# Kernel tuning notes

Hardware: AMD Instinct MI355X
Metric: run time of the kernel (lower is better)

## Reference

```python
import jax, jax.numpy as jnp
import numpy as np

DIM = 6
HID = 8
N_UT = DIM * (DIM - 1) // 2  # 15


def setup_inputs() -> dict:
    key = jax.random.key(0)
    ks = jax.random.split(key, 13)
    B, T = 256, 4096
    x = jax.random.normal(ks[0], (B, T, DIM), dtype=jnp.float32)

    def kaiming(k, fan_out, fan_in):
        std = np.sqrt(2.0 / fan_in)
        return jax.random.normal(k, (fan_out, fan_in), dtype=jnp.float32) * std

    inp = {
        "x": x,
        "W_in": kaiming(ks[1], HID, DIM),
        "b_in": jnp.zeros((HID,), jnp.float32),
        "W1": kaiming(ks[2], HID, HID), "b1": jnp.zeros((HID,), jnp.float32),
        "W2": kaiming(ks[3], HID, HID), "b2": jnp.zeros((HID,), jnp.float32),
        "W3": kaiming(ks[4], HID, HID), "b3": jnp.zeros((HID,), jnp.float32),
        "W4": kaiming(ks[5], HID, HID), "b4": jnp.zeros((HID,), jnp.float32),
        "W_out": kaiming(ks[6], N_UT, HID),
        "b_out": jnp.zeros((N_UT,), jnp.float32),
    }
    return inp


def reference(x, W_in, b_in, W1, b1, W2, b2, W3, b3, W4, b4, W_out, b_out):
    B, T, dim = x.shape
    xf = x.reshape(B * T, dim)
    sp = jax.nn.softplus
    y = sp(xf @ W_in.T + b_in)
    y = sp(y @ W1.T + b1)
    y = sp(y @ W2.T + b2)
    y = sp(y @ W3.T + b3)
    y = sp(y @ W4.T + b4)
    ut = y @ W_out.T + b_out  # [N, dim*(dim-1)/2]
    iu, ju = jnp.triu_indices(dim, k=1)  # row-major order matches torch loop
    L = jnp.zeros((B * T, dim, dim), dtype=x.dtype)
    L = L.at[:, iu, ju].set(ut)
    L = L.at[:, ju, iu].set(-ut)
    return L.reshape(B, T, dim, dim)
```

## Files before the change

### kernel.cpp

```cpp
#include <hip/hip_runtime.h>

#define DEV_INLINE __device__ __forceinline__

DEV_INLINE float softplus_f(float v) {
    return fmaxf(v, 0.0f) + __logf(1.0f + __expf(-fabsf(v)));
}

__global__ __launch_bounds__(256) void pb_kernel(
    const float* __restrict__ x,
    const float* __restrict__ W_in, const float* __restrict__ b_in,
    const float* __restrict__ W1,   const float* __restrict__ b1,
    const float* __restrict__ W2,   const float* __restrict__ b2,
    const float* __restrict__ W3,   const float* __restrict__ b3,
    const float* __restrict__ W4,   const float* __restrict__ b4,
    const float* __restrict__ W_out,const float* __restrict__ b_out,
    float* __restrict__ out, int n_rows)
{
    __shared__ float4 sbuf[256 * 9];

    const int tid = threadIdx.x;
    const int row_raw = blockIdx.x * 256 + tid;
    const int row = row_raw < n_rows ? row_raw : n_rows - 1;

    const float2* xv = (const float2*)(x + (size_t)row * 6);
    float2 p0 = xv[0], p1 = xv[1], p2 = xv[2];
    const float xin[6] = { p0.x, p0.y, p1.x, p1.y, p2.x, p2.y };

    float y[8];
    #pragma unroll
    for (int o = 0; o < 8; ++o) {
        float acc = b_in[o];
        #pragma unroll
        for (int i = 0; i < 6; ++i)
            acc = fmaf(W_in[o * 6 + i], xin[i], acc);
        y[o] = softplus_f(acc);
    }

    const float* Ws[4] = { W1, W2, W3, W4 };
    const float* bs[4] = { b1, b2, b3, b4 };
    #pragma unroll
    for (int l = 0; l < 4; ++l) {
        const float* __restrict__ W = Ws[l];
        const float* __restrict__ b = bs[l];
        float t[8];
        #pragma unroll
        for (int o = 0; o < 8; ++o) {
            float acc = b[o];
            #pragma unroll
            for (int i = 0; i < 8; ++i)
                acc = fmaf(W[o * 8 + i], y[i], acc);
            t[o] = softplus_f(acc);
        }
        #pragma unroll
        for (int o = 0; o < 8; ++o) y[o] = t[o];
    }

    float u[15];
    #pragma unroll
    for (int o = 0; o < 15; ++o) {
        float acc = b_out[o];
        #pragma unroll
        for (int i = 0; i < 8; ++i)
            acc = fmaf(W_out[o * 8 + i], y[i], acc);
        u[o] = acc;
    }

    float L[36];
    #pragma unroll
    for (int i = 0; i < 36; ++i) L[i] = 0.0f;
    {
        int k = 0;
        #pragma unroll
        for (int i = 0; i < 6; ++i) {
            #pragma unroll
            for (int j = i + 1; j < 6; ++j) {
                L[i * 6 + j] = u[k];
                L[j * 6 + i] = -u[k];
                ++k;
            }
        }
    }

    #pragma unroll
    for (int m = 0; m < 9; ++m)
        sbuf[tid * 9 + m] = make_float4(L[4 * m + 0], L[4 * m + 1],
                                        L[4 * m + 2], L[4 * m + 3]);

    __syncthreads();

    float4* dst = (float4*)out + (size_t)blockIdx.x * (256 * 9);
    const long long total_f4 = (long long)n_rows * 9;
    #pragma unroll
    for (int q = 0; q < 9; ++q) {
        const int idx = q * 256 + tid;
        const long long gidx = (long long)blockIdx.x * (256 * 9) + idx;
        if (gidx < total_f4)
            dst[idx] = sbuf[idx];
    }
}

extern "C" void kernel_launch(void* const* d_in, const int* in_sizes, int n_in,
                              void* d_out, int out_size, void* d_ws, size_t ws_size,
                              hipStream_t stream) {
    const float* x     = (const float*)d_in[0];
    const float* W_in  = (const float*)d_in[1];
    const float* b_in  = (const float*)d_in[2];
    const float* W1    = (const float*)d_in[3];
    const float* b1    = (const float*)d_in[4];
    const float* W2    = (const float*)d_in[5];
    const float* b2    = (const float*)d_in[6];
    const float* W3    = (const float*)d_in[7];
    const float* b3    = (const float*)d_in[8];
    const float* W4    = (const float*)d_in[9];
    const float* b4    = (const float*)d_in[10];
    const float* W_out = (const float*)d_in[11];
    const float* b_out = (const float*)d_in[12];
    float* out = (float*)d_out;

    const int n_rows = in_sizes[0] / 6;
    const int block = 256;
    const int grid = (n_rows + block - 1) / block;

    hipLaunchKernelGGL(pb_kernel, dim3(grid), dim3(block), 0, stream,
                       x, W_in, b_in, W1, b1, W2, b2, W3, b3, W4, b4,
                       W_out, b_out, out, n_rows);
}
```

Baseline: 197.2 us.

## Use per-wave LDS staging, nontemporal stores, and native exp2/log softplus

Splits the shared staging buffer into one slice per wavefront, so each wave transposes its own 64 rows and only waits on its own LDS writes instead of a block-wide barrier. The output is written with nontemporal stores so the large write stream does not pollute the cache. Softplus now calls the hardware exp2/log builtins with base conversion to avoid the extra work in __expf/__logf. The bounds check on the output is removed, which assumes the row count is a multiple of 256. Relying on an s_waitcnt with no barrier assumes intra-wave lockstep, which is fragile.

```diff
diff --git a/kernel.cpp b/kernel.cpp
--- a/kernel.cpp
+++ b/kernel.cpp
@@ -2,8 +2,16 @@
 
 #define DEV_INLINE __device__ __forceinline__
 
+typedef float vfloat4 __attribute__((ext_vector_type(4)));
+
 DEV_INLINE float softplus_f(float v) {
+#if __has_builtin(__builtin_amdgcn_logf) && __has_builtin(__builtin_amdgcn_exp2f)
+    float e = __builtin_amdgcn_exp2f(fabsf(v) * -1.44269504f);
+    float l = __builtin_amdgcn_logf(1.0f + e);
+    return fmaf(0.69314718f, l, fmaxf(v, 0.0f));
+#else
     return fmaxf(v, 0.0f) + __logf(1.0f + __expf(-fabsf(v)));
+#endif
 }
 
 __global__ __launch_bounds__(256) void pb_kernel(
@@ -16,9 +24,11 @@
     const float* __restrict__ W_out,const float* __restrict__ b_out,
     float* __restrict__ out, int n_rows)
 {
-    __shared__ float4 sbuf[256 * 9];
+    __shared__ vfloat4 sbuf[4][64 * 9];
 
-    const int tid = threadIdx.x;
+    const int tid  = threadIdx.x;
+    const int wave = tid >> 6;
+    const int lane = tid & 63;
     const int row_raw = blockIdx.x * 256 + tid;
     const int row = row_raw < n_rows ? row_raw : n_rows - 1;
 
@@ -81,21 +91,20 @@
         }
     }
 
+    vfloat4* ws = sbuf[wave];
     #pragma unroll
-    for (int m = 0; m < 9; ++m)
-        sbuf[tid * 9 + m] = make_float4(L[4 * m + 0], L[4 * m + 1],
-                                        L[4 * m + 2], L[4 * m + 3]);
+    for (int m = 0; m < 9; ++m) {
+        vfloat4 v = { L[4 * m + 0], L[4 * m + 1], L[4 * m + 2], L[4 * m + 3] };
+        ws[lane * 9 + m] = v;
+    }
 
-    __syncthreads();
+    asm volatile("s_waitcnt lgkmcnt(0)" ::: "memory");
 
-    float4* dst = (float4*)out + (size_t)blockIdx.x * (256 * 9);
-    const long long total_f4 = (long long)n_rows * 9;
+    vfloat4* dst = (vfloat4*)out + (size_t)blockIdx.x * (256 * 9) + wave * (64 * 9);
     #pragma unroll
     for (int q = 0; q < 9; ++q) {
-        const int idx = q * 256 + tid;
-        const long long gidx = (long long)blockIdx.x * (256 * 9) + idx;
-        if (gidx < total_f4)
-            dst[idx] = sbuf[idx];
+        vfloat4 v = ws[q * 64 + lane];
+        __builtin_nontemporal_store(v, &dst[q * 64 + lane]);
     }
 }
 
```

New measurement: 198.9 us. Within noise of the previous version (+0.9%).
